# Optimization experiments

Measured on AMD Instinct MI355X. Metric: run time of the kernel, lower is better.

Reference implementation:

```python
import jax, jax.numpy as jnp
import numpy as np

B, N, C, K = 64, 32768, 2, 10   # batch, num predictions, num classes, padded GT slots (build_target default N=10)
VL = 1.0e6                      # 'very_large' sentinel from torch code
EPS = 1e-08
W_LOC = W_CLASS = W_CONF = 1.0


def setup_inputs() -> dict:
    key = jax.random.key(0)
    k1, k2, k3, k4, k5, k6, k7 = jax.random.split(key, 7)
    p_start = jax.random.normal(k1, (B, N), dtype=jnp.float32)
    p_end = jax.random.normal(k2, (B, N), dtype=jnp.float32)
    p_class_logits = jax.random.normal(k3, (B, N, C), dtype=jnp.float32)
    p_conf_logits = jax.random.normal(k4, (B, N), dtype=jnp.float32)
    # GT intervals in [0,1] (compared against sigmoid(pred)); class channel in {0,1}
    fs = jax.random.uniform(k5, (B, K), dtype=jnp.float32)
    fe = jnp.clip(fs + 0.2 * jax.random.uniform(k6, (B, K), dtype=jnp.float32), 0.0, 1.0)
    cls = jax.random.randint(k7, (B, K), 0, C).astype(jnp.float32)
    gt_boxes = jnp.stack([fs, fe, cls], axis=-1)  # (B, K, 3)
    return {'p_start': p_start, 'p_end': p_end, 'p_class_logits': p_class_logits,
            'p_conf_logits': p_conf_logits, 'gt_boxes': gt_boxes}


def _build_target(gt_boxes):
    fs, fe, cls = gt_boxes[..., 0], gt_boxes[..., 1], gt_boxes[..., 2]
    presence = (~(jnp.isnan(fs) | jnp.isnan(fe) | jnp.isnan(cls))).astype(jnp.float32)
    fs = jnp.nan_to_num(fs)
    fe = jnp.nan_to_num(fe)
    cls = jnp.nan_to_num(cls)
    onehot = jax.nn.one_hot(jnp.clip(cls.astype(jnp.int32), 0, C - 1), C, dtype=jnp.float32)
    return fs, fe, onehot, presence


def _match_and_losses(cost, ps, pe, pcl, pconf, fs, fe, onehot):
    # cost: (K, N); greedy one-to-one argmin matching with row/col masking.
    Kp, Np = cost.shape

    def step(c, _):
        flat = c.reshape(-1)
        idx = jnp.argmin(flat)
        val = flat[idx]
        row, col = idx // Np, idx % Np
        valid = val < VL / 2
        c = c.at[row, :].set(VL).at[:, col].set(VL)
        return c, (row, col, valid)

    _, (rows, cols, valids) = jax.lax.scan(step, jax.lax.stop_gradient(cost), None, length=Kp)
    vm = valids.astype(jnp.float32)  # (K,)

    sel_s = jax.nn.sigmoid(ps[cols])
    sel_e = jax.nn.sigmoid(pe[cols])
    gs, ge = fs[rows], fe[rows]
    loc = (sel_s - gs) ** 2 + (sel_e - ge) ** 2

    logits = pcl[cols]          # (K, C)
    y = onehot[rows]            # (K, C)
    bce = (y * jax.nn.softplus(-logits) + (1.0 - y) * jax.nn.softplus(logits)).sum(-1)

    # IoU target is computed from .item() values in torch -> constant (no grad)
    ss, se = jax.lax.stop_gradient(sel_s), jax.lax.stop_gradient(sel_e)
    gss, gse = jax.lax.stop_gradient(gs), jax.lax.stop_gradient(ge)
    a1, b1 = jnp.minimum(ss, se), jnp.maximum(ss, se)
    a2, b2 = jnp.minimum(gss, gse), jnp.maximum(gss, gse)
    inter = jnp.maximum(0.0, jnp.minimum(b1, b2) - jnp.maximum(a1, a2))
    union = jnp.maximum(EPS, jnp.maximum(b1, b2) - jnp.minimum(a1, a2))
    iou = inter / union
    conf = (jax.nn.sigmoid(pconf[cols]) - iou) ** 2

    return (loc * vm).sum(), (bce * vm).sum(), (conf * vm).sum(), vm.sum()


def reference(p_start, p_end, p_class_logits, p_conf_logits, gt_boxes):
    fs, fe, onehot, presence = _build_target(gt_boxes)  # (B,K), (B,K), (B,K,C), (B,K)
    ps_sig = jax.nn.sigmoid(p_start)
    pe_sig = jax.nn.sigmoid(p_end)
    # loc MSE cost: (B, K, N)
    loc = (ps_sig[:, None, :] - fs[:, :, None]) ** 2 + (pe_sig[:, None, :] - fe[:, :, None]) ** 2
    # class L2 cost without materializing (B,K,N,C): |a-b|^2 = |a|^2 - 2 a.b + |b|^2
    sc = jax.nn.sigmoid(p_class_logits)  # (B, N, C)
    class_l2 = ((sc ** 2).sum(-1)[:, None, :]
                - 2.0 * jnp.einsum('bnc,bkc->bkn', sc, onehot)
                + (onehot ** 2).sum(-1)[:, :, None])
    cost = loc + class_l2
    # invalid (absent) GT rows get sentinel cost so greedy skips them
    cost = jnp.where(presence[:, :, None] > 0, cost, VL)

    loc_s, cls_s, conf_s, m = jax.vmap(_match_and_losses)(
        cost, p_start, p_end, p_class_logits, p_conf_logits, fs, fe, onehot)

    total_m = m.sum()
    denom = total_m + EPS
    total = (W_LOC * loc_s.sum() + W_CLASS * cls_s.sum() + W_CONF * conf_s.sum()) / denom
    return jnp.where(total_m > 0, total, 0.0)
```

## Files before the change

kernel.cpp:

```cpp
#include <hip/hip_runtime.h>
#include <cfloat>
#include <cmath>

#define BB 64
#define NN 32768
#define CC 2
#define KK 10
#define S_SL 64
#define SLICE (NN / S_SL)
#define TPM 256
#define VLARGE 1.0e6
#define KEY32_MAX 0xFFFFFFFFu
#define VMASK 0xFFFFFC00u
#define CMASK 0x3FFu
#define BND_MARGIN 1.0e-3

__device__ __forceinline__ double dsig(float x) { return 1.0 / (1.0 + exp(-(double)x)); }
__device__ __forceinline__ double dsoftplus(double x) {
    return fmax(x, 0.0) + log1p(exp(-fabs(x)));
}
__device__ __forceinline__ float rdfl_f(float x) {
    return __int_as_float(__builtin_amdgcn_readfirstlane(__float_as_int(x)));
}
__device__ __forceinline__ void merge2_32(unsigned& a1, unsigned& a2,
                                          unsigned b1, unsigned b2) {
    unsigned lo = a1 < b1 ? a1 : b1;
    unsigned hi = a1 < b1 ? b1 : a1;
    unsigned mb = a2 < b2 ? a2 : b2;
    a2 = hi < mb ? hi : mb;
    a1 = lo;
}
__device__ __forceinline__ void colterms(float sraw, float eraw, float q0raw, float q1raw,
                                         float& s, float& e, float& u0, float& u1) {
    s = __fdividef(1.0f, 1.0f + __expf(-sraw));
    e = __fdividef(1.0f, 1.0f + __expf(-eraw));
    const float q0 = __fdividef(1.0f, 1.0f + __expf(-q0raw));
    const float q1 = __fdividef(1.0f, 1.0f + __expf(-q1raw));
    const float se2 = fmaf(s, s, e * e);
    const float t0 = q0 - 1.0f, t1 = q1 - 1.0f;
    u0 = se2 + fmaf(t0, t0, q1 * q1);
    u1 = se2 + fmaf(t1, t1, q0 * q0);
}
__device__ __forceinline__ float rowcost(float s, float e, float u0, float u1,
                                         float m0, float m1, float ckv, int cls) {
    float c = fmaf(m0, s, fmaf(m1, e, ((cls == 0) ? u0 : u1) + ckv));
    return fmaxf(c, 0.0f);
}
__device__ __forceinline__ double eval64(const float* ps, const float* pe, const float* pc,
                                         double fs, double fe, int cls, int pres, int col) {
    if (!pres) return VLARGE;
    const double s  = dsig(ps[col]);
    const double e  = dsig(pe[col]);
    const double q0 = dsig(pc[2 * col]);
    const double q1 = dsig(pc[2 * col + 1]);
    const double d0 = s - fs, d1 = e - fe;
    const double sc = (cls == 0) ? q0 : q1;
    return d0 * d0 + d1 * d1 + (q0 * q0 + q1 * q1 - 2.0 * sc + 1.0);
}

__global__ __launch_bounds__(64)
void scan_kernel(const float* __restrict__ p_start, const float* __restrict__ p_end,
                 const float* __restrict__ p_cls, const float* __restrict__ gt,
                 uint2* __restrict__ cand) {
    const int sl = blockIdx.x, b = blockIdx.y, lane = threadIdx.x;
    const float2* ps2 = (const float2*)(p_start + (size_t)b * NN);
    const float2* pe2 = (const float2*)(p_end   + (size_t)b * NN);
    const float4* pc4 = (const float4*)(p_cls   + (size_t)b * NN * CC);

    float2 SV[4], EV[4]; float4 CV[4];
    const int base2 = sl * (SLICE / 2);
    #pragma unroll
    for (int it = 0; it < 4; it++) {
        const int pidx = base2 + it * 64 + lane;
        SV[it] = ps2[pidx]; EV[it] = pe2[pidx]; CV[it] = pc4[pidx];
    }

    float m0[KK], m1[KK], ck[KK]; int rcl[KK];
    #pragma unroll
    for (int k = 0; k < KK; k++) {
        float f0 = gt[((size_t)b * KK + k) * 3 + 0];
        float f1 = gt[((size_t)b * KK + k) * 3 + 1];
        float f2 = gt[((size_t)b * KK + k) * 3 + 2];
        int pres = !(isnan(f0) || isnan(f1) || isnan(f2));
        if (isnan(f0)) f0 = 0.0f;
        if (isnan(f1)) f1 = 0.0f;
        if (isnan(f2)) f2 = 0.0f;
        int ci = (int)f2; ci = ci < 0 ? 0 : (ci > CC - 1 ? CC - 1 : ci);
        m0[k] = rdfl_f(-2.0f * f0);
        m1[k] = rdfl_f(-2.0f * f1);
        ck[k] = rdfl_f(fmaf(f0, f0, f1 * f1) + (pres ? 0.0f : (float)VLARGE));
        rcl[k] = __builtin_amdgcn_readfirstlane(ci);
    }

    unsigned k1[KK], k2[KK];
    #pragma unroll
    for (int k = 0; k < KK; k++) { k1[k] = KEY32_MAX; k2[k] = KEY32_MAX; }

    #pragma unroll
    for (int it = 0; it < 4; it++) {
        #pragma unroll
        for (int h = 0; h < 2; h++) {
            const unsigned colLocal = 2u * (it * 64 + lane) + h;
            float s, e, u0, u1;
            colterms(h ? SV[it].y : SV[it].x, h ? EV[it].y : EV[it].x,
                     h ? CV[it].z : CV[it].x, h ? CV[it].w : CV[it].y, s, e, u0, u1);
            #pragma unroll
            for (int k = 0; k < KK; k++) {
                const float cost = rowcost(s, e, u0, u1, m0[k], m1[k], ck[k], rcl[k]);
                const unsigned key = (__float_as_uint(cost) & VMASK) | colLocal;
                if (key < k2[k]) {
                    if (key < k1[k]) { k2[k] = k1[k]; k1[k] = key; }
                    else             { k2[k] = key; }
                }
            }
        }
    }

    #pragma unroll
    for (int off = 1; off < 64; off <<= 1) {
        #pragma unroll
        for (int k = 0; k < KK; k++) {
            const unsigned o1 = __shfl_xor(k1[k], off, 64);
            const unsigned o2 = __shfl_xor(k2[k], off, 64);
            merge2_32(k1[k], k2[k], o1, o2);
        }
    }
    #pragma unroll
    for (int k = 0; k < KK; k++) {
        if (lane == k) {
            uint2 pk; pk.x = k1[k]; pk.y = k2[k];
            cand[((size_t)b * S_SL + sl) * KK + k] = pk;
        }
    }
}

__global__ __launch_bounds__(TPM)
void match_kernel(const float* __restrict__ p_start, const float* __restrict__ p_end,
                  const float* __restrict__ p_cls, const float* __restrict__ p_conf,
                  const float* __restrict__ gt, const uint2* __restrict__ cand,
                  double* __restrict__ partials, unsigned int* __restrict__ counter,
                  float* __restrict__ out, int out_size) {
    const int b = blockIdx.x, tid = threadIdx.x;
    const int j = tid & 63, wv = tid >> 6;
    const float* ps  = p_start + (size_t)b * NN;
    const float* pe  = p_end   + (size_t)b * NN;
    const float* pc  = p_cls   + (size_t)b * NN * CC;
    const float* pcf = p_conf  + (size_t)b * NN;

    __shared__ double l_cost[KK][2 * S_SL];
    __shared__ int    l_col[KK][2 * S_SL];
    __shared__ double l_bnd[KK][S_SL];
    __shared__ double gfs[KK], gfe[KK];
    __shared__ int    gcls[KK], gpres[KK];

    if (tid < KK) {
        float f0 = gt[((size_t)b * KK + tid) * 3 + 0];
        float f1 = gt[((size_t)b * KK + tid) * 3 + 1];
        float f2 = gt[((size_t)b * KK + tid) * 3 + 2];
        int pres = !(isnan(f0) || isnan(f1) || isnan(f2));
        if (isnan(f0)) f0 = 0.0f;
        if (isnan(f1)) f1 = 0.0f;
        if (isnan(f2)) f2 = 0.0f;
        int ci = (int)f2; ci = ci < 0 ? 0 : (ci > CC - 1 ? CC - 1 : ci);
        gfs[tid] = (double)f0; gfe[tid] = (double)f1;
        gcls[tid] = ci; gpres[tid] = pres;
    }
    __syncthreads();

    for (int idx = tid; idx < KK * 2 * S_SL; idx += TPM) {
        const int r = idx >> 7, jj = idx & 127, sl = jj >> 1;
        uint2 pk = cand[((size_t)b * S_SL + sl) * KK + r];
        const unsigned key = (jj & 1) ? pk.y : pk.x;
        int c = sl * SLICE + (int)(key & CMASK);
        if (c < 0 || c >= NN) c = 0;
        l_cost[r][jj] = eval64(ps, pe, pc, gfs[r], gfe[r], gcls[r], gpres[r], c);
        l_col[r][jj]  = c;
        if (jj & 1)
            l_bnd[r][sl] = (double)__uint_as_float(key & VMASK) - BND_MARGIN;
    }
    __syncthreads();
    if (wv != 0) return;

    double v0[KK], v1v[KK], bnd[KK]; int c0[KK], c1v[KK];
    #pragma unroll
    for (int r = 0; r < KK; r++) {
        v0[r] = l_cost[r][2 * j];     c0[r]  = l_col[r][2 * j];
        v1v[r] = l_cost[r][2 * j + 1]; c1v[r] = l_col[r][2 * j + 1];
        bnd[r] = l_bnd[r][j];
    }

    unsigned act = (1u << KK) - 1;
    int cons[KK], prow[KK], pcolv[KK], pvalid[KK];
    #pragma unroll
    for (int r = 0; r < KK; r++) { cons[r] = -1; pvalid[r] = 0; prow[r] = 0; pcolv[r] = 0; }

    for (int step = 0; step < KK; step++) {
        double bv = DBL_MAX; int brow = 0x7fffffff, bcol = 0x7fffffff;
        for (int guard = 0; guard < 64; guard++) {
            double lv = DBL_MAX; int lr = 0x7fffffff, lc = 0x7fffffff;
            #pragma unroll
            for (int r = 0; r < KK; r++) {
                if (!((act >> r) & 1)) continue;
                const bool a0 = (c0[r] >= 0), a1 = (c1v[r] >= 0);
                double va = DBL_MAX; int ca = 0x7fffffff;
                if (a0) { va = v0[r]; ca = c0[r]; }
                if (a1 && (v1v[r] < va || (v1v[r] == va && c1v[r] < ca))) { va = v1v[r]; ca = c1v[r]; }
                if (!a0 && !a1 && bnd[r] < DBL_MAX) { va = bnd[r]; ca = -2 - j; }
                if (va < lv || (va == lv && (r < lr || (r == lr && ca < lc)))) {
                    lv = va; lr = r; lc = ca;
                }
            }
            #pragma unroll
            for (int off = 1; off < 64; off <<= 1) {
                const double ov = __shfl_xor(lv, off, 64);
                const int   orr = __shfl_xor(lr, off, 64);
                const int   oc  = __shfl_xor(lc, off, 64);
                if (ov < lv || (ov == lv && (orr < lr || (orr == lr && oc < lc)))) {
                    lv = ov; lr = orr; lc = oc;
                }
            }
            bv = lv; brow = lr; bcol = lc;
            if (bcol >= 0 || bv == DBL_MAX) break;

            const int ss = -2 - bcol;
            const float ffs = (float)gfs[brow], ffe = (float)gfe[brow];
            const int   cb  = gcls[brow], pb = gpres[brow];
            const float m0b = -2.0f * ffs, m1b = -2.0f * ffe;
            const float ckb = fmaf(ffs, ffs, ffe * ffe) + (pb ? 0.0f : (float)VLARGE);
            unsigned q1 = KEY32_MAX, q2 = KEY32_MAX;
            const int cbase = ss * SLICE;
            for (int t = j; t < SLICE; t += 64) {
                const int n = cbase + t;
                bool used = false;
                #pragma unroll
                for (int u = 0; u < KK; u++) used |= (cons[u] == n);
                float s, e, u0, u1;
                colterms(ps[n], pe[n], pc[2 * n], pc[2 * n + 1], s, e, u0, u1);
                const float cst = rowcost(s, e, u0, u1, m0b, m1b, ckb, cb);
                const unsigned kk = used ? KEY32_MAX : ((__float_as_uint(cst) & VMASK) | (unsigned)t);
                if (kk < q2) { if (kk < q1) { q2 = q1; q1 = kk; } else { q2 = kk; } }
            }
            #pragma unroll
            for (int off = 1; off < 64; off <<= 1) {
                const unsigned o1 = __shfl_xor(q1, off, 64);
                const unsigned o2 = __shfl_xor(q2, off, 64);
                merge2_32(q1, q2, o1, o2);
            }
            int cA = cbase + (int)(q1 & CMASK);
            int cB = cbase + (int)(q2 & CMASK);
            if (cA < 0 || cA >= NN) cA = 0;
            if (cB < 0 || cB >= NN) cB = 0;
            const double vA = (q1 == KEY32_MAX) ? DBL_MAX
                : eval64(ps, pe, pc, gfs[brow], gfe[brow], cb, pb, cA);
            const double vB = (q2 == KEY32_MAX) ? DBL_MAX
                : eval64(ps, pe, pc, gfs[brow], gfe[brow], cb, pb, cB);
            const double nb = (q2 == KEY32_MAX) ? DBL_MAX
                : (double)__uint_as_float(q2 & VMASK) - BND_MARGIN;
            #pragma unroll
            for (int r = 0; r < KK; r++) {
                if (r != brow) continue;
                if (j == ss) {
                    v0[r]  = vA; c0[r]  = (q1 == KEY32_MAX) ? -1 : cA;
                    v1v[r] = vB; c1v[r] = (q2 == KEY32_MAX) ? -1 : cB;
                    bnd[r] = nb;
                }
            }
        }

        prow[step]   = brow;
        pcolv[step]  = bcol;
        pvalid[step] = (bv < VLARGE * 0.5) && (bcol >= 0) && (brow < KK);
        cons[step]   = (bcol >= 0) ? bcol : -1;
        if (brow < KK) act &= ~(1u << brow);
        else break;

        if (bcol >= 0) {
            #pragma unroll
            for (int r = 0; r < KK; r++) {
                if (c0[r] == bcol)  { c0[r] = -1;  v0[r]  = DBL_MAX; }
                if (c1v[r] == bcol) { c1v[r] = -1; v1v[r] = DBL_MAX; }
            }
        }
    }

    double loss = 0.0, m = 0.0;
    if (j < KK && pvalid[j]) {
        const int r = prow[j], cidx = pcolv[j];
        const double ss = dsig(ps[cidx]);
        const double se = dsig(pe[cidx]);
        const double gs = gfs[r], ge = gfe[r];
        const double d0 = ss - gs, d1 = se - ge;
        double acc = d0 * d0 + d1 * d1;

        const double l0 = (double)pc[2 * cidx];
        const double l1 = (double)pc[2 * cidx + 1];
        const double y0 = (gcls[r] == 0) ? 1.0 : 0.0;
        const double y1 = 1.0 - y0;
        acc += y0 * dsoftplus(-l0) + (1.0 - y0) * dsoftplus(l0)
             + y1 * dsoftplus(-l1) + (1.0 - y1) * dsoftplus(l1);

        const double a1 = fmin(ss, se), b1 = fmax(ss, se);
        const double a2 = fmin(gs, ge), b2 = fmax(gs, ge);
        const double inter = fmax(0.0, fmin(b1, b2) - fmax(a1, a2));
        const double uni   = fmax(1e-8, fmax(b1, b2) - fmin(a1, a2));
        const double iou   = inter / uni;
        const double dcf   = dsig(pcf[cidx]) - iou;
        acc += dcf * dcf;
        loss = acc; m = 1.0;
    }
    #pragma unroll
    for (int off = 1; off < 64; off <<= 1) {
        loss += __shfl_xor(loss, off, 64);
        m    += __shfl_xor(m, off, 64);
    }
    if (j == 0) { partials[b * 2 + 0] = loss; partials[b * 2 + 1] = m; }

    __threadfence();
    int ticket = 0;
    if (j == 0) ticket = (int)atomicAdd(counter, 1u);
    ticket = __shfl(ticket, 0, 64);
    if (ticket == BB - 1) {
        __threadfence();
        for (int i = j; i < out_size; i += 64) out[i] = 0.0f;
        double s = partials[j * 2 + 0];
        double mm = partials[j * 2 + 1];
        #pragma unroll
        for (int off = 1; off < 64; off <<= 1) {
            s  += __shfl_xor(s, off, 64);
            mm += __shfl_xor(mm, off, 64);
        }
        if (j == 0) {
            const double total = s / (mm + 1e-8);
            out[0] = (float)(mm > 0.0 ? total : 0.0);
        }
    }
}

extern "C" void kernel_launch(void* const* d_in, const int* in_sizes, int n_in,
                              void* d_out, int out_size, void* d_ws, size_t ws_size,
                              hipStream_t stream) {
    const float* p_start = (const float*)d_in[0];
    const float* p_end   = (const float*)d_in[1];
    const float* p_cls   = (const float*)d_in[2];
    const float* p_conf  = (const float*)d_in[3];
    const float* gt      = (const float*)d_in[4];

    const size_t cand_bytes = (size_t)BB * S_SL * KK * sizeof(uint2);
    const size_t part_bytes = (size_t)BB * 2 * sizeof(double);
    uint2*        cand     = (uint2*)d_ws;
    double*       partials = (double*)((char*)d_ws + cand_bytes);
    unsigned int* counter  = (unsigned int*)((char*)d_ws + cand_bytes + part_bytes);

    hipMemsetAsync(counter, 0, sizeof(unsigned int), stream);
    scan_kernel<<<dim3(S_SL, BB), 64, 0, stream>>>(p_start, p_end, p_cls, gt, cand);
    match_kernel<<<BB, TPM, 0, stream>>>(p_start, p_end, p_cls, p_conf, gt, cand,
                                         partials, counter, (float*)d_out, out_size);
}
```

Baseline: 144.4 us.

## Lazily evaluate second candidate costs and fold counter reset into scan kernel

The match kernel now evaluates the exact double-precision cost only for the best candidate per slice and row up front. The second candidate is kept as a lower bound and evaluated on demand through a new lazy-evaluation event in the greedy loop, which halves the initial eval64 work and its scattered global loads. The hipMemsetAsync that cleared the counter is replaced by a write from the first thread of scan_kernel, removing one launch. In exchange the guard loop can run more iterations (limit raised to 256), each lazy event costs a full wave reduction, and the counter reset now depends on kernel ordering.

After: 141.8 us. No clear change (-1.8%).

```diff
diff --git a/kernel.cpp b/kernel.cpp
--- a/kernel.cpp
+++ b/kernel.cpp
@@ -61,8 +61,9 @@
 __global__ __launch_bounds__(64)
 void scan_kernel(const float* __restrict__ p_start, const float* __restrict__ p_end,
                  const float* __restrict__ p_cls, const float* __restrict__ gt,
-                 uint2* __restrict__ cand) {
+                 uint2* __restrict__ cand, unsigned int* __restrict__ counter) {
     const int sl = blockIdx.x, b = blockIdx.y, lane = threadIdx.x;
+    if (sl == 0 && b == 0 && lane == 0) *counter = 0;
     const float2* ps2 = (const float2*)(p_start + (size_t)b * NN);
     const float2* pe2 = (const float2*)(p_end   + (size_t)b * NN);
     const float4* pc4 = (const float4*)(p_cls   + (size_t)b * NN * CC);
@@ -147,8 +148,9 @@
     const float* pc  = p_cls   + (size_t)b * NN * CC;
     const float* pcf = p_conf  + (size_t)b * NN;
 
-    __shared__ double l_cost[KK][2 * S_SL];
-    __shared__ int    l_col[KK][2 * S_SL];
+    __shared__ double l_cost[KK][S_SL];
+    __shared__ int    l_col[KK][S_SL];
+    __shared__ int    l_col2[KK][S_SL];
     __shared__ double l_bnd[KK][S_SL];
     __shared__ double gfs[KK], gfe[KK];
     __shared__ int    gcls[KK], gpres[KK];
@@ -167,26 +169,25 @@
     }
     __syncthreads();
 
-    for (int idx = tid; idx < KK * 2 * S_SL; idx += TPM) {
-        const int r = idx >> 7, jj = idx & 127, sl = jj >> 1;
+    for (int idx = tid; idx < KK * S_SL; idx += TPM) {
+        const int r = idx >> 6, sl = idx & 63;
         uint2 pk = cand[((size_t)b * S_SL + sl) * KK + r];
-        const unsigned key = (jj & 1) ? pk.y : pk.x;
-        int c = sl * SLICE + (int)(key & CMASK);
+        int c = sl * SLICE + (int)(pk.x & CMASK);
         if (c < 0 || c >= NN) c = 0;
-        l_cost[r][jj] = eval64(ps, pe, pc, gfs[r], gfe[r], gcls[r], gpres[r], c);
-        l_col[r][jj]  = c;
-        if (jj & 1)
-            l_bnd[r][sl] = (double)__uint_as_float(key & VMASK) - BND_MARGIN;
+        l_cost[r][sl] = eval64(ps, pe, pc, gfs[r], gfe[r], gcls[r], gpres[r], c);
+        l_col[r][sl]  = c;
+        l_col2[r][sl] = sl * SLICE + (int)(pk.y & CMASK);
+        l_bnd[r][sl]  = (double)__uint_as_float(pk.y & VMASK) - BND_MARGIN;
     }
     __syncthreads();
     if (wv != 0) return;
 
-    double v0[KK], v1v[KK], bnd[KK]; int c0[KK], c1v[KK];
+    double v0[KK], v2[KK], bnd[KK]; int c0[KK], c1[KK];
+    unsigned e2bits = 0;
     #pragma unroll
     for (int r = 0; r < KK; r++) {
-        v0[r] = l_cost[r][2 * j];     c0[r]  = l_col[r][2 * j];
-        v1v[r] = l_cost[r][2 * j + 1]; c1v[r] = l_col[r][2 * j + 1];
-        bnd[r] = l_bnd[r][j];
+        v0[r] = l_cost[r][j]; c0[r] = l_col[r][j];
+        c1[r] = l_col2[r][j]; bnd[r] = l_bnd[r][j]; v2[r] = bnd[r];
     }
 
     unsigned act = (1u << KK) - 1;
@@ -196,16 +197,21 @@
 
     for (int step = 0; step < KK; step++) {
         double bv = DBL_MAX; int brow = 0x7fffffff, bcol = 0x7fffffff;
-        for (int guard = 0; guard < 64; guard++) {
+        for (int guard = 0; guard < 256; guard++) {
             double lv = DBL_MAX; int lr = 0x7fffffff, lc = 0x7fffffff;
             #pragma unroll
             for (int r = 0; r < KK; r++) {
                 if (!((act >> r) & 1)) continue;
-                const bool a0 = (c0[r] >= 0), a1 = (c1v[r] >= 0);
+                const bool a0 = (c0[r] >= 0), a1 = (c1[r] >= 0);
+                const bool ev = (e2bits >> r) & 1;
                 double va = DBL_MAX; int ca = 0x7fffffff;
                 if (a0) { va = v0[r]; ca = c0[r]; }
-                if (a1 && (v1v[r] < va || (v1v[r] == va && c1v[r] < ca))) { va = v1v[r]; ca = c1v[r]; }
-                if (!a0 && !a1 && bnd[r] < DBL_MAX) { va = bnd[r]; ca = -2 - j; }
+                if (a1) {
+                    const double vb = ev ? v2[r] : bnd[r];
+                    const int    cb2 = ev ? c1[r] : (-2 - 2 * j);
+                    if (vb < va || (vb == va && cb2 < ca)) { va = vb; ca = cb2; }
+                }
+                if (!a0 && !a1 && bnd[r] < DBL_MAX) { va = bnd[r]; ca = -3 - 2 * j; }
                 if (va < lv || (va == lv && (r < lr || (r == lr && ca < lc)))) {
                     lv = va; lr = r; lc = ca;
                 }
@@ -222,7 +228,21 @@
             bv = lv; brow = lr; bcol = lc;
             if (bcol >= 0 || bv == DBL_MAX) break;
 
-            const int ss = -2 - bcol;
+            const int idxn = -bcol - 2;
+            const int ss = idxn >> 1, kind = idxn & 1;
+
+            if (kind == 0) {
+                #pragma unroll
+                for (int r = 0; r < KK; r++) {
+                    if (r != brow) continue;
+                    int cc = __shfl(c1[r], ss, 64);
+                    if (cc < 0 || cc >= NN) cc = 0;
+                    const double vv = eval64(ps, pe, pc, gfs[r], gfe[r], gcls[r], gpres[r], cc);
+                    if (j == ss) { v2[r] = vv; e2bits |= (1u << r); }
+                }
+                continue;
+            }
+
             const float ffs = (float)gfs[brow], ffe = (float)gfe[brow];
             const int   cb  = gcls[brow], pb = gpres[brow];
             const float m0b = -2.0f * ffs, m1b = -2.0f * ffe;
@@ -260,8 +280,9 @@
             for (int r = 0; r < KK; r++) {
                 if (r != brow) continue;
                 if (j == ss) {
-                    v0[r]  = vA; c0[r]  = (q1 == KEY32_MAX) ? -1 : cA;
-                    v1v[r] = vB; c1v[r] = (q2 == KEY32_MAX) ? -1 : cB;
+                    v0[r] = vA; c0[r] = (q1 == KEY32_MAX) ? -1 : cA;
+                    v2[r] = vB; c1[r] = (q2 == KEY32_MAX) ? -1 : cB;
+                    e2bits |= (1u << r);
                     bnd[r] = nb;
                 }
             }
@@ -277,8 +298,8 @@
         if (bcol >= 0) {
             #pragma unroll
             for (int r = 0; r < KK; r++) {
-                if (c0[r] == bcol)  { c0[r] = -1;  v0[r]  = DBL_MAX; }
-                if (c1v[r] == bcol) { c1v[r] = -1; v1v[r] = DBL_MAX; }
+                if (c0[r] == bcol) { c0[r] = -1; v0[r] = DBL_MAX; }
+                if (c1[r] == bcol) { c1[r] = -1; }
             }
         }
     }
@@ -351,8 +372,7 @@
     double*       partials = (double*)((char*)d_ws + cand_bytes);
     unsigned int* counter  = (unsigned int*)((char*)d_ws + cand_bytes + part_bytes);
 
-    hipMemsetAsync(counter, 0, sizeof(unsigned int), stream);
-    scan_kernel<<<dim3(S_SL, BB), 64, 0, stream>>>(p_start, p_end, p_cls, gt, cand);
+    scan_kernel<<<dim3(S_SL, BB), 64, 0, stream>>>(p_start, p_end, p_cls, gt, cand, counter);
     match_kernel<<<BB, TPM, 0, stream>>>(p_start, p_end, p_cls, p_conf, gt, cand,
                                          partials, counter, (float*)d_out, out_size);
 }
```
